# Performance work log

Measured on AMD Instinct MI355X. Metric: run time of the kernel, lower is better.

The kernel has to match this reference:

```python
import jax, jax.numpy as jnp
import numpy as np

INPUT_SIZE = 20
HIDDEN = 51
OUT = 1
B = 4096
T = 512


def _init_lstm_params(key, in_dim, hid_dim):
    # PyTorch LSTMCell init: U(-1/sqrt(hid), 1/sqrt(hid))
    k = 1.0 / np.sqrt(hid_dim)
    ks = jax.random.split(key, 4)
    W_ih = jax.random.uniform(ks[0], (4 * hid_dim, in_dim), minval=-k, maxval=k, dtype=jnp.float32)
    W_hh = jax.random.uniform(ks[1], (4 * hid_dim, hid_dim), minval=-k, maxval=k, dtype=jnp.float32)
    b_ih = jax.random.uniform(ks[2], (4 * hid_dim,), minval=-k, maxval=k, dtype=jnp.float32)
    b_hh = jax.random.uniform(ks[3], (4 * hid_dim,), minval=-k, maxval=k, dtype=jnp.float32)
    return W_ih, W_hh, b_ih, b_hh


def setup_inputs() -> dict:
    key = jax.random.key(0)
    k_x, k1, k2, k3, k4 = jax.random.split(key, 5)
    x = jax.random.normal(k_x, (B, T, INPUT_SIZE), dtype=jnp.float32)
    W_ih1, W_hh1, b_ih1, b_hh1 = _init_lstm_params(k1, INPUT_SIZE, HIDDEN)
    W_ih2, W_hh2, b_ih2, b_hh2 = _init_lstm_params(k2, HIDDEN, OUT)
    kl = 1.0 / np.sqrt(OUT)
    ka, kb, kc, kd = jax.random.split(k3, 4)
    W_mu = jax.random.uniform(ka, (OUT, OUT), minval=-kl, maxval=kl, dtype=jnp.float32)
    b_mu = jax.random.uniform(kb, (OUT,), minval=-kl, maxval=kl, dtype=jnp.float32)
    W_lv = jax.random.uniform(kc, (OUT, OUT), minval=-kl, maxval=kl, dtype=jnp.float32)
    b_lv = jax.random.uniform(kd, (OUT,), minval=-kl, maxval=kl, dtype=jnp.float32)
    return {
        "x": x,
        "W_ih1": W_ih1, "W_hh1": W_hh1, "b_ih1": b_ih1, "b_hh1": b_hh1,
        "W_ih2": W_ih2, "W_hh2": W_hh2, "b_ih2": b_ih2, "b_hh2": b_hh2,
        "W_mu": W_mu, "b_mu": b_mu, "W_lv": W_lv, "b_lv": b_lv,
    }


def _lstm_cell(x_t, h, c, W_ih, W_hh, b_ih, b_hh):
    # PyTorch LSTMCell: gate order i, f, g, o
    gates = x_t @ W_ih.T + b_ih + h @ W_hh.T + b_hh
    i, f, g, o = jnp.split(gates, 4, axis=-1)
    c_new = jax.nn.sigmoid(f) * c + jax.nn.sigmoid(i) * jnp.tanh(g)
    h_new = jax.nn.sigmoid(o) * jnp.tanh(c_new)
    return h_new, c_new


def reference(x, W_ih1, W_hh1, b_ih1, b_hh1, W_ih2, W_hh2, b_ih2, b_hh2, W_mu, b_mu, W_lv, b_lv):
    bsz = x.shape[0]
    h1 = jnp.zeros((bsz, HIDDEN), dtype=x.dtype)
    c1 = jnp.zeros((bsz, HIDDEN), dtype=x.dtype)
    h2 = jnp.zeros((bsz, OUT), dtype=x.dtype)
    c2 = jnp.zeros((bsz, OUT), dtype=x.dtype)

    def step(carry, x_t):
        h1, c1, h2, c2 = carry
        h1, c1 = _lstm_cell(x_t, h1, c1, W_ih1, W_hh1, b_ih1, b_hh1)
        h2, c2 = _lstm_cell(h1, h2, c2, W_ih2, W_hh2, b_ih2, b_hh2)
        return (h1, c1, h2, c2), h2

    xs = jnp.swapaxes(x, 0, 1)  # [T, B, input_size]
    _, h2_seq = jax.lax.scan(step, (h1, c1, h2, c2), xs)  # h2_seq: [T, B, 1]
    agg = jnp.mean(h2_seq, axis=0)  # [B, 1] mean over time
    mu = agg @ W_mu.T + b_mu
    log_var = agg @ W_lv.T + b_lv
    sigma = jnp.exp(0.5 * log_var)
    lower = mu - 1.96 * sigma
    upper = mu + 1.96 * sigma
    return (lower, mu, upper, log_var)
```

## Files before the change

### kernel.cpp

```cpp
#include <hip/hip_runtime.h>

#define B_TOT 4096
#define T_STEPS 512
#define IN 20
#define HID 51

typedef float f32x4 __attribute__((ext_vector_type(4)));
typedef short s16x8 __attribute__((ext_vector_type(8)));

__device__ __forceinline__ unsigned short f2bf(float f) {
    unsigned int u = __float_as_uint(f);
    unsigned int r = (u + 0x7fffu + ((u >> 16) & 1u)) >> 16;
    return (unsigned short)r;
}

__device__ __forceinline__ float fast_rcp(float x) { return __builtin_amdgcn_rcpf(x); }
__device__ __forceinline__ float sigf(float x) { return fast_rcp(1.0f + __expf(-x)); }
__device__ __forceinline__ float tanh_(float x) { return 1.0f - 2.0f * fast_rcp(1.0f + __expf(2.0f * x)); }


__global__ __launch_bounds__(256, 1)
void lstm_fused(const float* __restrict__ x,
                const float* __restrict__ Wih1, const float* __restrict__ Whh1,
                const float* __restrict__ bih1, const float* __restrict__ bhh1,
                const float* __restrict__ Wih2, const float* __restrict__ Whh2,
                const float* __restrict__ bih2, const float* __restrict__ bhh2,
                const float* __restrict__ Wmu,  const float* __restrict__ bmu,
                const float* __restrict__ Wlv,  const float* __restrict__ blv,
                float* __restrict__ out)
{
    __shared__ __align__(16) unsigned short vA[2][3][64][8];

    const int tid  = threadIdx.x;
    const int lane = tid & 63;
    const int w    = tid >> 6;
    const int bidx = blockIdx.x;

    const int tbase = (w < 3) ? 3 * w : 9;
    const int ntile = (w < 3) ? 3 : 4;
    const bool isST = (w == 0);
    const bool isL2 = (w == 2);

    s16x8 wfrag[4][3];
    f32x4 binit[4];
    #pragma unroll
    for (int ti = 0; ti < 4; ++ti) {
        const int tau = tbase + ti;
        const int m = lane & 15;
        const bool act = (ti < ntile);
        #pragma unroll
        for (int ks = 0; ks < 3; ++ks) {
            s16x8 f;
            #pragma unroll
            for (int j = 0; j < 8; ++j) {
                int k = ks * 32 + ((lane >> 4) << 3) + j;
                float v = 0.0f;
                if (act) {
                    int g = m & 3, unit = tau * 4 + (m >> 2);
                    if (unit < HID) {
                        int row = g * HID + unit;
                        if (k < IN) v = Wih1[row * IN + k];
                        else if (k >= 32 && k < 32 + HID) v = Whh1[row * HID + (k - 32)];
                    }
                }
                f[j] = (short)f2bf(v);
            }
            wfrag[ti][ks] = f;
        }
        f32x4 bi = {0.f, 0.f, 0.f, 0.f};
        if (act) {
            int unit = tau * 4 + (lane >> 4);
            if (unit < HID) {
                #pragma unroll
                for (int r = 0; r < 4; ++r) bi[r] = bih1[r * HID + unit] + bhh1[r * HID + unit];
            }
        }
        binit[ti] = bi;
    }

    s16x8 l2frag[2];
    f32x4 l2binit = {0.f, 0.f, 0.f, 0.f};
    float whh2g[4];
    if (isL2) {
        const int m = lane & 15;
        #pragma unroll
        for (int ks = 1; ks < 3; ++ks) {
            s16x8 f;
            #pragma unroll
            for (int j = 0; j < 8; ++j) {
                int k = ks * 32 + ((lane >> 4) << 3) + j;
                float v = 0.0f;
                if (m < 4 && k >= 32 && k < 32 + HID) v = Wih2[m * HID + (k - 32)];
                f[j] = (short)f2bf(v);
            }
            l2frag[ks - 1] = f;
        }
        #pragma unroll
        for (int r = 0; r < 4; ++r) { whh2g[r] = Whh2[r]; l2binit[r] = bih2[r] + bhh2[r]; }
    }

    const float* sp[5];
    int srow[5], sj[5];
    if (isST) {
        #pragma unroll
        for (int i = 0; i < 5; ++i) {
            int e = i * 64 + lane;
            int b = e / IN, m = e % IN;
            sp[i]   = x + ((size_t)(bidx * 16 + b) * T_STEPS) * IN + m;
            srow[i] = ((m >> 3) & 3) * 16 + b;
            sj[i]   = m & 7;
        }
    }

    {
        unsigned short* vz = &vA[0][0][0][0];
        for (int i = tid; i < 2 * 3 * 64 * 8; i += 256) vz[i] = 0;
    }
    __syncthreads();
    float xr[5];
    if (isST) {
        #pragma unroll
        for (int i = 0; i < 5; ++i) {
            vA[0][0][srow[i]][sj[i]] = f2bf(sp[i][0]);
            xr[i] = sp[i][IN];
        }
    }
    __syncthreads();

    float c1[4] = {0.f, 0.f, 0.f, 0.f};
    float c2p = 0.f, h2p = 0.f, sum2 = 0.f;

    for (int t = 0; t < T_STEPS; ++t) {
        const int p  = t & 1;
        const int pn = p ^ 1;

        s16x8 bf0 = *(const s16x8*)&vA[p][0][lane][0];
        s16x8 bf1 = *(const s16x8*)&vA[p][1][lane][0];
        s16x8 bf2 = *(const s16x8*)&vA[p][2][lane][0];

        #pragma unroll
        for (int ti = 0; ti < 4; ++ti) {
            if (ti < ntile) {
                f32x4 a = binit[ti];
                a = __builtin_amdgcn_mfma_f32_16x16x32_bf16(wfrag[ti][0], bf0, a, 0, 0, 0);
                a = __builtin_amdgcn_mfma_f32_16x16x32_bf16(wfrag[ti][1], bf1, a, 0, 0, 0);
                a = __builtin_amdgcn_mfma_f32_16x16x32_bf16(wfrag[ti][2], bf2, a, 0, 0, 0);

                float c = sigf(a[1]) * c1[ti] + sigf(a[0]) * tanh_(a[2]);
                c1[ti] = c;
                float h = sigf(a[3]) * tanh_(c);
                int unit = (tbase + ti) * 4 + (lane >> 4);
                int k    = 32 + unit;
                int b    = lane & 15;
                vA[pn][k >> 5][(((k >> 3) & 3) << 4) + b][k & 7] = f2bf(h);
            }
        }

        if (isL2) {
            f32x4 a = l2binit;
            a = __builtin_amdgcn_mfma_f32_16x16x32_bf16(l2frag[0], bf1, a, 0, 0, 0);
            a = __builtin_amdgcn_mfma_f32_16x16x32_bf16(l2frag[1], bf2, a, 0, 0, 0);
            if (t > 0 && lane < 16) {
                float pi = a[0] + whh2g[0] * h2p;
                float pf = a[1] + whh2g[1] * h2p;
                float pg = a[2] + whh2g[2] * h2p;
                float po = a[3] + whh2g[3] * h2p;
                float c2 = sigf(pf) * c2p + sigf(pi) * tanh_(pg);
                c2p = c2;
                h2p = sigf(po) * tanh_(c2);
                sum2 += h2p;
            }
        }

        if (isST) {
            const int t2 = (t < T_STEPS - 2) ? t + 2 : T_STEPS - 1;
            #pragma unroll
            for (int i = 0; i < 5; ++i) {
                vA[pn][0][srow[i]][sj[i]] = f2bf(xr[i]);
                xr[i] = sp[i][(size_t)t2 * IN];
            }
        }

        __syncthreads();
    }

    if (isL2) {
        s16x8 bf1 = *(const s16x8*)&vA[0][1][lane][0];
        s16x8 bf2 = *(const s16x8*)&vA[0][2][lane][0];
        f32x4 a = l2binit;
        a = __builtin_amdgcn_mfma_f32_16x16x32_bf16(l2frag[0], bf1, a, 0, 0, 0);
        a = __builtin_amdgcn_mfma_f32_16x16x32_bf16(l2frag[1], bf2, a, 0, 0, 0);
        if (lane < 16) {
            float pi = a[0] + whh2g[0] * h2p;
            float pf = a[1] + whh2g[1] * h2p;
            float pg = a[2] + whh2g[2] * h2p;
            float po = a[3] + whh2g[3] * h2p;
            float c2 = sigf(pf) * c2p + sigf(pi) * tanh_(pg);
            h2p = sigf(po) * tanh_(c2);
            sum2 += h2p;

            float agg = sum2 * (1.0f / 512.0f);
            float mu  = Wmu[0] * agg + bmu[0];
            float lv  = Wlv[0] * agg + blv[0];
            float sg  = __expf(0.5f * lv);
            int bg = bidx * 16 + lane;
            out[bg]             = mu - 1.96f * sg;
            out[B_TOT + bg]     = mu;
            out[2 * B_TOT + bg] = mu + 1.96f * sg;
            out[3 * B_TOT + bg] = lv;
        }
    }
}

extern "C" void kernel_launch(void* const* d_in, const int* in_sizes, int n_in,
                              void* d_out, int out_size, void* d_ws, size_t ws_size,
                              hipStream_t stream) {
    const float* x    = (const float*)d_in[0];
    const float* Wih1 = (const float*)d_in[1];
    const float* Whh1 = (const float*)d_in[2];
    const float* bih1 = (const float*)d_in[3];
    const float* bhh1 = (const float*)d_in[4];
    const float* Wih2 = (const float*)d_in[5];
    const float* Whh2 = (const float*)d_in[6];
    const float* bih2 = (const float*)d_in[7];
    const float* bhh2 = (const float*)d_in[8];
    const float* Wmu  = (const float*)d_in[9];
    const float* bmu  = (const float*)d_in[10];
    const float* Wlv  = (const float*)d_in[11];
    const float* blv  = (const float*)d_in[12];
    float* out = (float*)d_out;

    lstm_fused<<<dim3(B_TOT / 16), dim3(256), 0, stream>>>(
        x, Wih1, Whh1, bih1, bhh1, Wih2, Whh2, bih2, bhh2, Wmu, bmu, Wlv, blv, out);
}
```

Baseline: 504.9 us.

## Spread LSTM tiles over 8 waves, prescale gates by log2e, unroll steps by two

Doubles the block to 512 threads (8 waves) so each wave handles at most two 16x16 gate tiles instead of three or four. This shortens the per-step critical path of the serial recurrence. Weights and biases are prescaled by -log2(e) or 2*log2(e), so the activations use exp2 directly without a multiply. The time loop is unrolled by two with compile-time double-buffer parity. In exchange there are more waves per block sharing each barrier, and prescaling before bf16 rounding slightly changes numerics.

Measured after the change: 505.4 us. About the same (+0.1%).

```diff
diff --git a/kernel.cpp b/kernel.cpp
--- a/kernel.cpp
+++ b/kernel.cpp
@@ -14,12 +14,15 @@
     return (unsigned short)r;
 }
 
+#define L2E  1.4426950408889634f
+#define L2E2 2.8853900817779268f
+
 __device__ __forceinline__ float fast_rcp(float x) { return __builtin_amdgcn_rcpf(x); }
-__device__ __forceinline__ float sigf(float x) { return fast_rcp(1.0f + __expf(-x)); }
-__device__ __forceinline__ float tanh_(float x) { return 1.0f - 2.0f * fast_rcp(1.0f + __expf(2.0f * x)); }
-
-
-__global__ __launch_bounds__(256, 1)
+__device__ __forceinline__ float sig_p(float p) { return fast_rcp(1.0f + exp2f(p)); }
+__device__ __forceinline__ float tanh_q(float q) { return 1.0f - 2.0f * fast_rcp(1.0f + exp2f(q)); }
+
+
+__global__ __launch_bounds__(512, 2)
 void lstm_fused(const float* __restrict__ x,
                 const float* __restrict__ Wih1, const float* __restrict__ Whh1,
                 const float* __restrict__ bih1, const float* __restrict__ bhh1,
@@ -36,15 +39,15 @@
     const int w    = tid >> 6;
     const int bidx = blockIdx.x;
 
-    const int tbase = (w < 3) ? 3 * w : 9;
-    const int ntile = (w < 3) ? 3 : 4;
+    const int tbase = (w == 0) ? 0 : (w == 7) ? 12 : 2 * w - 1;
+    const int ntile = (w >= 1 && w <= 5) ? 2 : 1;
     const bool isST = (w == 0);
-    const bool isL2 = (w == 2);
-
-    s16x8 wfrag[4][3];
-    f32x4 binit[4];
+    const bool isL2 = (w == 6);
+
+    s16x8 wfrag[2][3];
+    f32x4 binit[2];
     #pragma unroll
-    for (int ti = 0; ti < 4; ++ti) {
+    for (int ti = 0; ti < 2; ++ti) {
         const int tau = tbase + ti;
         const int m = lane & 15;
         const bool act = (ti < ntile);
@@ -61,6 +64,7 @@
                         int row = g * HID + unit;
                         if (k < IN) v = Wih1[row * IN + k];
                         else if (k >= 32 && k < 32 + HID) v = Whh1[row * HID + (k - 32)];
+                        v *= (g == 2) ? L2E2 : -L2E;
                     }
                 }
                 f[j] = (short)f2bf(v);
@@ -72,7 +76,8 @@
             int unit = tau * 4 + (lane >> 4);
             if (unit < HID) {
                 #pragma unroll
-                for (int r = 0; r < 4; ++r) bi[r] = bih1[r * HID + unit] + bhh1[r * HID + unit];
+                for (int r = 0; r < 4; ++r)
+                    bi[r] = (bih1[r * HID + unit] + bhh1[r * HID + unit]) * ((r == 2) ? L2E2 : -L2E);
             }
         }
         binit[ti] = bi;
@@ -80,7 +85,7 @@
 
     s16x8 l2frag[2];
     f32x4 l2binit = {0.f, 0.f, 0.f, 0.f};
-    float whh2g[4];
+    float whh2g[4] = {0.f, 0.f, 0.f, 0.f};
     if (isL2) {
         const int m = lane & 15;
         #pragma unroll
@@ -90,13 +95,18 @@
             for (int j = 0; j < 8; ++j) {
                 int k = ks * 32 + ((lane >> 4) << 3) + j;
                 float v = 0.0f;
-                if (m < 4 && k >= 32 && k < 32 + HID) v = Wih2[m * HID + (k - 32)];
+                if (m < 4 && k >= 32 && k < 32 + HID)
+                    v = Wih2[m * HID + (k - 32)] * ((m == 2) ? L2E2 : -L2E);
                 f[j] = (short)f2bf(v);
             }
             l2frag[ks - 1] = f;
         }
         #pragma unroll
-        for (int r = 0; r < 4; ++r) { whh2g[r] = Whh2[r]; l2binit[r] = bih2[r] + bhh2[r]; }
+        for (int r = 0; r < 4; ++r) {
+            float s = (r == 2) ? L2E2 : -L2E;
+            whh2g[r]   = Whh2[r] * s;
+            l2binit[r] = (bih2[r] + bhh2[r]) * s;
+        }
     }
 
     const float* sp[5];
@@ -114,7 +124,7 @@
 
     {
         unsigned short* vz = &vA[0][0][0][0];
-        for (int i = tid; i < 2 * 3 * 64 * 8; i += 256) vz[i] = 0;
+        for (int i = tid; i < 2 * 3 * 64 * 8; i += 512) vz[i] = 0;
     }
     __syncthreads();
     float xr[5];
@@ -127,62 +137,61 @@
     }
     __syncthreads();
 
-    float c1[4] = {0.f, 0.f, 0.f, 0.f};
+    float c1[2] = {0.f, 0.f};
     float c2p = 0.f, h2p = 0.f, sum2 = 0.f;
 
-    for (int t = 0; t < T_STEPS; ++t) {
-        const int p  = t & 1;
-        const int pn = p ^ 1;
-
-        s16x8 bf0 = *(const s16x8*)&vA[p][0][lane][0];
-        s16x8 bf1 = *(const s16x8*)&vA[p][1][lane][0];
-        s16x8 bf2 = *(const s16x8*)&vA[p][2][lane][0];
-
-        #pragma unroll
-        for (int ti = 0; ti < 4; ++ti) {
-            if (ti < ntile) {
-                f32x4 a = binit[ti];
-                a = __builtin_amdgcn_mfma_f32_16x16x32_bf16(wfrag[ti][0], bf0, a, 0, 0, 0);
-                a = __builtin_amdgcn_mfma_f32_16x16x32_bf16(wfrag[ti][1], bf1, a, 0, 0, 0);
-                a = __builtin_amdgcn_mfma_f32_16x16x32_bf16(wfrag[ti][2], bf2, a, 0, 0, 0);
-
-                float c = sigf(a[1]) * c1[ti] + sigf(a[0]) * tanh_(a[2]);
-                c1[ti] = c;
-                float h = sigf(a[3]) * tanh_(c);
-                int unit = (tbase + ti) * 4 + (lane >> 4);
-                int k    = 32 + unit;
-                int b    = lane & 15;
-                vA[pn][k >> 5][(((k >> 3) & 3) << 4) + b][k & 7] = f2bf(h);
-            }
-        }
-
-        if (isL2) {
-            f32x4 a = l2binit;
-            a = __builtin_amdgcn_mfma_f32_16x16x32_bf16(l2frag[0], bf1, a, 0, 0, 0);
-            a = __builtin_amdgcn_mfma_f32_16x16x32_bf16(l2frag[1], bf2, a, 0, 0, 0);
-            if (t > 0 && lane < 16) {
-                float pi = a[0] + whh2g[0] * h2p;
-                float pf = a[1] + whh2g[1] * h2p;
-                float pg = a[2] + whh2g[2] * h2p;
-                float po = a[3] + whh2g[3] * h2p;
-                float c2 = sigf(pf) * c2p + sigf(pi) * tanh_(pg);
-                c2p = c2;
-                h2p = sigf(po) * tanh_(c2);
-                sum2 += h2p;
-            }
-        }
-
-        if (isST) {
-            const int t2 = (t < T_STEPS - 2) ? t + 2 : T_STEPS - 1;
-            #pragma unroll
-            for (int i = 0; i < 5; ++i) {
-                vA[pn][0][srow[i]][sj[i]] = f2bf(xr[i]);
-                xr[i] = sp[i][(size_t)t2 * IN];
-            }
-        }
-
-        __syncthreads();
-    }
+#define STEP(P, tt)                                                              \
+    {                                                                            \
+        const s16x8 bf0 = *(const s16x8*)&vA[P][0][lane][0];                     \
+        const s16x8 bf1 = *(const s16x8*)&vA[P][1][lane][0];                     \
+        const s16x8 bf2 = *(const s16x8*)&vA[P][2][lane][0];                     \
+        _Pragma("unroll")                                                        \
+        for (int ti = 0; ti < 2; ++ti) {                                         \
+            if (ti < ntile) {                                                    \
+                f32x4 a = binit[ti];                                             \
+                a = __builtin_amdgcn_mfma_f32_16x16x32_bf16(wfrag[ti][0], bf0, a, 0, 0, 0); \
+                a = __builtin_amdgcn_mfma_f32_16x16x32_bf16(wfrag[ti][1], bf1, a, 0, 0, 0); \
+                a = __builtin_amdgcn_mfma_f32_16x16x32_bf16(wfrag[ti][2], bf2, a, 0, 0, 0); \
+                float c = sig_p(a[1]) * c1[ti] + sig_p(a[0]) * tanh_q(a[2]);     \
+                c1[ti] = c;                                                      \
+                float h = sig_p(a[3]) * tanh_q(L2E2 * c);                        \
+                int unit = (tbase + ti) * 4 + (lane >> 4);                       \
+                int k    = 32 + unit;                                            \
+                int b    = lane & 15;                                            \
+                vA[(P) ^ 1][k >> 5][(((k >> 3) & 3) << 4) + b][k & 7] = f2bf(h); \
+            }                                                                    \
+        }                                                                        \
+        if (isL2) {                                                              \
+            f32x4 a = l2binit;                                                   \
+            a = __builtin_amdgcn_mfma_f32_16x16x32_bf16(l2frag[0], bf1, a, 0, 0, 0); \
+            a = __builtin_amdgcn_mfma_f32_16x16x32_bf16(l2frag[1], bf2, a, 0, 0, 0); \
+            if ((tt) > 0 && lane < 16) {                                         \
+                float pi = a[0] + whh2g[0] * h2p;                                \
+                float pf = a[1] + whh2g[1] * h2p;                                \
+                float pg = a[2] + whh2g[2] * h2p;                                \
+                float po = a[3] + whh2g[3] * h2p;                                \
+                float c2 = sig_p(pf) * c2p + sig_p(pi) * tanh_q(pg);             \
+                c2p = c2;                                                        \
+                h2p = sig_p(po) * tanh_q(L2E2 * c2);                             \
+                sum2 += h2p;                                                     \
+            }                                                                    \
+        }                                                                        \
+        if (isST) {                                                              \
+            const int t2 = ((tt) < T_STEPS - 2) ? (tt) + 2 : T_STEPS - 1;        \
+            _Pragma("unroll")                                                    \
+            for (int i = 0; i < 5; ++i) {                                        \
+                vA[(P) ^ 1][0][srow[i]][sj[i]] = f2bf(xr[i]);                    \
+                xr[i] = sp[i][(size_t)t2 * IN];                                  \
+            }                                                                    \
+        }                                                                        \
+        __syncthreads();                                                         \
+    }
+
+    for (int t = 0; t < T_STEPS; t += 2) {
+        STEP(0, t)
+        STEP(1, t + 1)
+    }
+#undef STEP
 
     if (isL2) {
         s16x8 bf1 = *(const s16x8*)&vA[0][1][lane][0];
@@ -195,8 +204,8 @@
             float pf = a[1] + whh2g[1] * h2p;
             float pg = a[2] + whh2g[2] * h2p;
             float po = a[3] + whh2g[3] * h2p;
-            float c2 = sigf(pf) * c2p + sigf(pi) * tanh_(pg);
-            h2p = sigf(po) * tanh_(c2);
+            float c2 = sig_p(pf) * c2p + sig_p(pi) * tanh_q(pg);
+            h2p = sig_p(po) * tanh_q(L2E2 * c2);
             sum2 += h2p;
 
             float agg = sum2 * (1.0f / 512.0f);
@@ -230,6 +239,6 @@
     const float* blv  = (const float*)d_in[12];
     float* out = (float*)d_out;
 
-    lstm_fused<<<dim3(B_TOT / 16), dim3(256), 0, stream>>>(
+    lstm_fused<<<dim3(B_TOT / 16), dim3(512), 0, stream>>>(
         x, Wih1, Whh1, bih1, bhh1, Wih2, Whh2, bih2, bhh2, Wmu, bmu, Wlv, blv, out);
 }
```
